# Performance work log

Hardware: AMD Instinct MI355X
Metric: run time of the kernel (lower is better)

Reference implementation:

```python
import jax, jax.numpy as jnp
import numpy as np

N_CONN = 21  # n_connections


def setup_inputs() -> dict:
    key = jax.random.key(0)
    landmarks = jax.random.normal(key, (262144, N_CONN, 3), dtype=jnp.float32)
    return {"landmarks": landmarks}


def reference(landmarks) -> jnp.ndarray:
    # Faithful to the TF layer: connections = [(i, j) for i in range(n) for j in range(n)],
    # connection_vectors[k] = landmarks[:, j_k] - landmarks[:, i_k]; the loop only reads
    # indices k < n, which correspond to pairs (0, k), so v_k = p_k - p_0 (v_0 == 0).
    b, n = landmarks.shape[0], N_CONN
    v = landmarks[:, :n, :] - landmarks[:, :1, :]          # (b, n, d)
    dots = jnp.einsum("bid,bjd->bij", v, v)                 # (b, n, n)
    norms = jnp.linalg.norm(v, axis=-1)                     # (b, n)
    cos = dots / (norms[:, :, None] * norms[:, None, :])    # 0/0 -> nan for v_0
    ang = jnp.arccos(cos)                                   # (b, n, n)
    ang = jnp.where(jnp.isnan(ang), jnp.zeros_like(ang), ang)
    # TF concatenates n*n tensors of shape (batch,) along axis -1 (== axis 0),
    # yielding shape (n*n*batch,) ordered angle-major.
    return ang.reshape(b, n * n).T.reshape(-1)
```

## Files before the change

### kernel.cpp

```cpp
#include <hip/hip_runtime.h>

#define NCONN 21
#define TPB 128

__global__ __launch_bounds__(TPB) void pv_kernel(const float* __restrict__ in,
                                                 float* __restrict__ out,
                                                 int B) {
    __shared__ float lds[TPB * 63];
    const int tid = threadIdx.x;
    const long long blockBatch = (long long)blockIdx.x * TPB;

    const long long gBase  = blockBatch * 63;
    const long long totalF4 = ((long long)B * 63) >> 2;
    const float4* in4 = (const float4*)in;
    const long long gBase4 = gBase >> 2;
    float4* lds4 = (float4*)lds;
    #pragma unroll
    for (int it = 0; it < 16; ++it) {
        int t = tid + it * TPB;
        if (t < (TPB * 63) / 4) {
            long long g4 = gBase4 + t;
            if (g4 < totalF4) lds4[t] = in4[g4];
        }
    }
    __syncthreads();

    const long long bl = blockBatch + tid;
    if (bl >= B) return;
    const int b = (int)bl;
    float* base = lds + tid * 63;

    const float p0x = base[0], p0y = base[1], p0z = base[2];
    #pragma unroll
    for (int e = 1; e < NCONN; ++e) {
        float vx = base[3*e+0] - p0x;
        float vy = base[3*e+1] - p0y;
        float vz = base[3*e+2] - p0z;
        float d  = fmaf(vx, vx, fmaf(vy, vy, vz * vz));
        float r  = rsqrtf(d);
        base[3*e+0] = vx * r;
        base[3*e+1] = vy * r;
        base[3*e+2] = vz * r;
    }

    const size_t sB = (size_t)B;
    float* outb = out + b;

    #pragma unroll
    for (int k = 0; k < NCONN; ++k) outb[(size_t)k * sB] = 0.0f;

    #pragma unroll
    for (int cc = 0; cc < 2; ++cc) {
        const int i0 = 1 + cc * 10;
        float uix[10], uiy[10], uiz[10];
        #pragma unroll
        for (int q = 0; q < 10; ++q) {
            uix[q] = base[3*(i0+q)+0];
            uiy[q] = base[3*(i0+q)+1];
            uiz[q] = base[3*(i0+q)+2];
        }
        #pragma unroll
        for (int q = 0; q < 10; ++q)
            outb[(size_t)((i0+q)*NCONN) * sB] = 0.0f;

        for (int j = 1; j < NCONN; ++j) {
            const float ujx = base[3*j+0];
            const float ujy = base[3*j+1];
            const float ujz = base[3*j+2];
            #pragma unroll
            for (int q = 0; q < 10; ++q) {
                float c = fmaf(uix[q], ujx, fmaf(uiy[q], ujy, uiz[q] * ujz));
                c = fmaxf(fminf(c, 1.0f), -1.0f);
                float t = fabsf(c);
                float s = sqrtf(1.0f - t);
                float p = fmaf(t, -0.0187293f, 0.0742610f);
                p = fmaf(t, p, -0.2121144f);
                p = fmaf(t, p, 1.5707288f);
                float r = s * p;
                float ang = (c >= 0.0f) ? r : (3.14159265358979f - r);
                outb[(size_t)((i0+q)*NCONN + j) * sB] = ang;
            }
        }
    }
}

extern "C" void kernel_launch(void* const* d_in, const int* in_sizes, int n_in,
                              void* d_out, int out_size, void* d_ws, size_t ws_size,
                              hipStream_t stream) {
    const float* in = (const float*)d_in[0];
    float* out = (float*)d_out;
    const int B = in_sizes[0] / (NCONN * 3);
    const int grid = (B + TPB - 1) / TPB;
    hipLaunchKernelGGL(pv_kernel, dim3(grid), dim3(TPB), 0, stream, in, out, B);
}
```

Baseline: 523.6 us.

## Remap threads to emit float4 output stores with rotated, padded LDS rows

The block now covers 256 batch rows. Input is staged into LDS rows padded to 64 floats, with a per-row rotation meant to avoid bank conflicts. Work is then redistributed so each thread computes 4 consecutive batch entries for a subset of j, which turns the strided scalar global stores into 16-byte float4 stores. This trades extra index arithmetic, an extra barrier and lower register reuse of the u_i vectors for better write coalescing and vectorization.

```diff
diff --git a/kernel.cpp b/kernel.cpp
--- a/kernel.cpp
+++ b/kernel.cpp
@@ -1,84 +1,119 @@
 #include <hip/hip_runtime.h>
 
 #define NCONN 21
-#define TPB 128
+#define TPB 256
+#define BPB 256
 
-__global__ __launch_bounds__(TPB) void pv_kernel(const float* __restrict__ in,
-                                                 float* __restrict__ out,
-                                                 int B) {
-    __shared__ float lds[TPB * 63];
+__global__ __launch_bounds__(TPB, 2) void pv_kernel(const float* __restrict__ in,
+                                                    float* __restrict__ out,
+                                                    int B) {
+    __shared__ float lds[BPB * 64];
     const int tid = threadIdx.x;
-    const long long blockBatch = (long long)blockIdx.x * TPB;
+    const long long blockBatch = (long long)blockIdx.x * BPB;
 
-    const long long gBase  = blockBatch * 63;
+    const long long gBase4 = blockBatch * 63 / 4;
     const long long totalF4 = ((long long)B * 63) >> 2;
     const float4* in4 = (const float4*)in;
-    const long long gBase4 = gBase >> 2;
-    float4* lds4 = (float4*)lds;
     #pragma unroll
     for (int it = 0; it < 16; ++it) {
-        int t = tid + it * TPB;
-        if (t < (TPB * 63) / 4) {
-            long long g4 = gBase4 + t;
-            if (g4 < totalF4) lds4[t] = in4[g4];
+        int t4 = tid + it * TPB;
+        if (t4 < (BPB * 63) / 4) {
+            long long g4 = gBase4 + t4;
+            if (g4 < totalF4) {
+                float4 v = in4[g4];
+                float vals[4] = {v.x, v.y, v.z, v.w};
+                int f = 4 * t4;
+                #pragma unroll
+                for (int q = 0; q < 4; ++q) {
+                    int f2 = f + q;
+                    int r  = f2 / 63;
+                    int c  = f2 - r * 63;
+                    lds[r * 64 + ((c + (r >> 2)) & 63)] = vals[q];
+                }
+            }
         }
     }
     __syncthreads();
 
-    const long long bl = blockBatch + tid;
-    if (bl >= B) return;
-    const int b = (int)bl;
-    float* base = lds + tid * 63;
+    if (blockBatch + tid < B) {
+        float* row = lds + tid * 64;
+        const int rot = tid >> 2;
+        const float p0x = row[(0 + rot) & 63];
+        const float p0y = row[(1 + rot) & 63];
+        const float p0z = row[(2 + rot) & 63];
+        #pragma unroll
+        for (int e = 1; e < NCONN; ++e) {
+            const int s0 = (3 * e + 0 + rot) & 63;
+            const int s1 = (3 * e + 1 + rot) & 63;
+            const int s2 = (3 * e + 2 + rot) & 63;
+            float vx = row[s0] - p0x;
+            float vy = row[s1] - p0y;
+            float vz = row[s2] - p0z;
+            float d  = fmaf(vx, vx, fmaf(vy, vy, vz * vz));
+            float rr = rsqrtf(d);
+            row[s0] = vx * rr;
+            row[s1] = vy * rr;
+            row[s2] = vz * rr;
+        }
+    }
+    __syncthreads();
 
-    const float p0x = base[0], p0y = base[1], p0z = base[2];
-    #pragma unroll
-    for (int e = 1; e < NCONN; ++e) {
-        float vx = base[3*e+0] - p0x;
-        float vy = base[3*e+1] - p0y;
-        float vz = base[3*e+2] - p0z;
-        float d  = fmaf(vx, vx, fmaf(vy, vy, vz * vz));
-        float r  = rsqrtf(d);
-        base[3*e+0] = vx * r;
-        base[3*e+1] = vy * r;
-        base[3*e+2] = vz * r;
+    const int l = tid & 63;
+    const int w = tid >> 6;
+    const int rowb = 4 * l;
+    const long long remLL = B - blockBatch;
+    const int rem = (int)(remLL < BPB ? remLL : (long long)BPB);
+    const bool fullv = (rowb + 4 <= rem);
+    float* op = out + blockBatch + rowb;
+    const size_t sB = (size_t)B;
+
+    {
+        const float4 z4 = make_float4(0.f, 0.f, 0.f, 0.f);
+        for (int idx = w; idx < 41; idx += 4) {
+            const int p = (idx < 21) ? idx : (idx - 20) * NCONN;
+            float* dst = op + (size_t)p * sB;
+            if (fullv) {
+                *(float4*)dst = z4;
+            } else {
+                for (int k = 0; rowb + k < rem; ++k) dst[k] = 0.0f;
+            }
+        }
     }
 
-    const size_t sB = (size_t)B;
-    float* outb = out + b;
-
-    #pragma unroll
-    for (int k = 0; k < NCONN; ++k) outb[(size_t)k * sB] = 0.0f;
-
-    #pragma unroll
-    for (int cc = 0; cc < 2; ++cc) {
-        const int i0 = 1 + cc * 10;
-        float uix[10], uiy[10], uiz[10];
+    for (int i = 1; i < NCONN; ++i) {
+        float uix[4], uiy[4], uiz[4];
         #pragma unroll
-        for (int q = 0; q < 10; ++q) {
-            uix[q] = base[3*(i0+q)+0];
-            uiy[q] = base[3*(i0+q)+1];
-            uiz[q] = base[3*(i0+q)+2];
+        for (int k = 0; k < 4; ++k) {
+            const float* row = lds + (rowb + k) * 64;
+            uix[k] = row[(3 * i + 0 + l) & 63];
+            uiy[k] = row[(3 * i + 1 + l) & 63];
+            uiz[k] = row[(3 * i + 2 + l) & 63];
         }
-        #pragma unroll
-        for (int q = 0; q < 10; ++q)
-            outb[(size_t)((i0+q)*NCONN) * sB] = 0.0f;
-
-        for (int j = 1; j < NCONN; ++j) {
-            const float ujx = base[3*j+0];
-            const float ujy = base[3*j+1];
-            const float ujz = base[3*j+2];
+        const size_t pibase = (size_t)(i * NCONN) * sB;
+        for (int jc = 1; jc <= 17; jc += 4) {
+            const int j = jc + w;
+            float ang[4];
             #pragma unroll
-            for (int q = 0; q < 10; ++q) {
-                float c = fmaf(uix[q], ujx, fmaf(uiy[q], ujy, uiz[q] * ujz));
+            for (int k = 0; k < 4; ++k) {
+                const float* row = lds + (rowb + k) * 64;
+                const float ujx = row[(3 * j + 0 + l) & 63];
+                const float ujy = row[(3 * j + 1 + l) & 63];
+                const float ujz = row[(3 * j + 2 + l) & 63];
+                float c = fmaf(uix[k], ujx, fmaf(uiy[k], ujy, uiz[k] * ujz));
                 c = fmaxf(fminf(c, 1.0f), -1.0f);
                 float t = fabsf(c);
                 float s = sqrtf(1.0f - t);
                 float p = fmaf(t, -0.0187293f, 0.0742610f);
                 p = fmaf(t, p, -0.2121144f);
                 p = fmaf(t, p, 1.5707288f);
-                float r = s * p;
-                float ang = (c >= 0.0f) ? r : (3.14159265358979f - r);
-                outb[(size_t)((i0+q)*NCONN + j) * sB] = ang;
+                float rr = s * p;
+                ang[k] = (c >= 0.0f) ? rr : (3.14159265358979f - rr);
+            }
+            float* dst = op + pibase + (size_t)j * sB;
+            if (fullv) {
+                *(float4*)dst = make_float4(ang[0], ang[1], ang[2], ang[3]);
+            } else {
+                for (int k = 0; rowb + k < rem; ++k) dst[k] = ang[k];
             }
         }
     }
@@ -90,6 +125,6 @@
     const float* in = (const float*)d_in[0];
     float* out = (float*)d_out;
     const int B = in_sizes[0] / (NCONN * 3);
-    const int grid = (B + TPB - 1) / TPB;
+    const int grid = (B + BPB - 1) / BPB;
     hipLaunchKernelGGL(pv_kernel, dim3(grid), dim3(TPB), 0, stream, in, out, B);
 }
```

Result: no change. 517.2 us (-1.2%).
